# Optimization experiments

Measured on AMD Instinct MI355X. Metric: run time of the kernel, lower is better.

## Reference

```python
import jax, jax.numpy as jnp
import numpy as np

NOISE_LEVEL = 0.02
CROSSTALK = 0.05
COHERENCE = 0.03
HIDDEN = 2048


def _crosstalk_kernel(n):
    # K[i, j] = 1 / (i - j)^2 for i != j, 0 on the diagonal
    idx = jnp.arange(n, dtype=jnp.float32)
    dist = jnp.abs(idx[:, None] - idx[None, :])
    return jnp.where(dist > 0, 1.0 / (dist * dist), 0.0)


def setup_inputs() -> dict:
    key = jax.random.key(0)
    ks = jax.random.split(key, 7)
    B, D_in, H, D_out = 8192, 1024, 2048, 2
    x = jax.random.normal(ks[0], (B, D_in), dtype=jnp.float32)
    # torch nn.Linear-like init scale: 1/sqrt(fan_in)
    W1 = jax.random.normal(ks[1], (H, D_in), dtype=jnp.float32) / np.sqrt(D_in)
    b1 = jax.random.normal(ks[2], (H,), dtype=jnp.float32) / np.sqrt(D_in)
    W2 = jax.random.normal(ks[3], (H, H), dtype=jnp.float32) / np.sqrt(H)
    b2 = jax.random.normal(ks[4], (H,), dtype=jnp.float32) / np.sqrt(H)
    Wout = jax.random.normal(ks[5], (D_out, H), dtype=jnp.float32) / np.sqrt(H)
    bout = jax.random.normal(ks[6], (D_out,), dtype=jnp.float32) / np.sqrt(H)
    return {"x": x, "W1": W1, "b1": b1, "W2": W2, "b2": b2, "Wout": Wout, "bout": bout}


def reference(x, W1, b1, W2, b2, Wout, bout):
    K = _crosstalk_kernel(HIDDEN)
    thermal = jnp.zeros((HIDDEN,), dtype=x.dtype)  # thermal_state buffer, carries across layers
    nkey = jax.random.key(42)

    x = jnp.tanh(x)
    for li, (W, b) in enumerate([(W1, b1), (W2, b2)]):
        x = jnp.tanh(x @ W.T + b)
        # physical noise (add_noise=True, training mode)
        k_noise = jax.random.fold_in(nkey, 2 * li)
        k_phase = jax.random.fold_in(nkey, 2 * li + 1)
        x = x + jax.random.normal(k_noise, x.shape, x.dtype) * NOISE_LEVEL
        # thermal crosstalk: EMA of per-neuron absolute power, then
        # distance-weighted (1/d^2) coupling — the O(n^2) python loop as a matvec
        layer_thermal = jnp.sum(jnp.abs(x), axis=0) * CROSSTALK  # [H]
        thermal = 0.7 * thermal + 0.3 * layer_thermal
        thermal_noise = (thermal @ K) * CROSSTALK  # [H], constant across batch
        x = x + thermal_noise[None, :]
        # coherence (phase-dependent interference)
        phase = jax.random.normal(k_phase, x.shape, x.dtype) * COHERENCE
        x = x + (x * jnp.cos(phase) - x) * COHERENCE
    return x @ Wout.T + bout
```

## Files before the change

### kernel.cpp

```cpp
#include <hip/hip_runtime.h>
#include <stdint.h>
#include <math.h>

#define NOISE_LEVEL 0.02f
#define CROSSTALK   0.05f
#define COHERENCE   0.03f
#define F_COH 0.99998650f

typedef _Float16 half8 __attribute__((ext_vector_type(8)));
typedef _Float16 half4 __attribute__((ext_vector_type(4)));
typedef __attribute__((ext_vector_type(4))) float f32x4;

#define TF_ROUND(x0,x1,R) { x0 += x1; x1 = ((x1 << (R)) | (x1 >> (32-(R)))); x1 ^= x0; }

__host__ __device__ inline void threefry2x32(uint32_t k0, uint32_t k1,
                                             uint32_t x0, uint32_t x1,
                                             uint32_t& o0, uint32_t& o1)
{
  uint32_t ks2 = k0 ^ k1 ^ 0x1BD11BDAu;
  x0 += k0; x1 += k1;
  TF_ROUND(x0,x1,13) TF_ROUND(x0,x1,15) TF_ROUND(x0,x1,26) TF_ROUND(x0,x1,6)
  x0 += k1; x1 += ks2 + 1u;
  TF_ROUND(x0,x1,17) TF_ROUND(x0,x1,29) TF_ROUND(x0,x1,16) TF_ROUND(x0,x1,24)
  x0 += ks2; x1 += k0 + 2u;
  TF_ROUND(x0,x1,13) TF_ROUND(x0,x1,15) TF_ROUND(x0,x1,26) TF_ROUND(x0,x1,6)
  x0 += k0; x1 += k1 + 3u;
  TF_ROUND(x0,x1,17) TF_ROUND(x0,x1,29) TF_ROUND(x0,x1,16) TF_ROUND(x0,x1,24)
  x0 += k1; x1 += ks2 + 4u;
  TF_ROUND(x0,x1,13) TF_ROUND(x0,x1,15) TF_ROUND(x0,x1,26) TF_ROUND(x0,x1,6)
  o0 = x0 + ks2; o1 = x1 + k0 + 5u;
}

__device__ inline uint32_t jax_bits(uint32_t k0, uint32_t k1, uint32_t idx)
{
  uint32_t o0, o1; threefry2x32(k0, k1, 0u, idx, o0, o1); return o0 ^ o1;
}

__device__ inline float jax_normal(uint32_t k0, uint32_t k1, uint32_t idx)
{
  uint32_t bits = jax_bits(k0, k1, idx);
  float f = __uint_as_float((bits >> 9) | 0x3f800000u) - 1.0f;
  float u = fmaf(f, 2.0f, -0.99999994f);
  u = fmaxf(-0.99999994f, u);
  float w = -__logf(fmaf(-u, u, 1.0f));
  float wl = w - 2.5f;
  float p = 2.81022636e-08f;
  p = fmaf(p, wl, 3.43273939e-07f);
  p = fmaf(p, wl, -3.5233877e-06f);
  p = fmaf(p, wl, -4.39150654e-06f);
  p = fmaf(p, wl, 0.00021858087f);
  p = fmaf(p, wl, -0.00125372503f);
  p = fmaf(p, wl, -0.00417768164f);
  p = fmaf(p, wl, 0.246640727f);
  p = fmaf(p, wl, 1.50140941f);
  if (__any(w >= 5.0f)) {
    float ws = sqrtf(w) - 3.0f;
    float q = -0.000200214257f;
    q = fmaf(q, ws, 0.000100950558f);
    q = fmaf(q, ws, 0.00134934322f);
    q = fmaf(q, ws, -0.00367342844f);
    q = fmaf(q, ws, 0.00573950773f);
    q = fmaf(q, ws, -0.0076224613f);
    q = fmaf(q, ws, 0.00943887047f);
    q = fmaf(q, ws, 1.00167406f);
    q = fmaf(q, ws, 2.83297682f);
    p = (w >= 5.0f) ? q : p;
  }
  return 1.41421354f * (p * u);
}

__device__ inline float tanh_fast(float x)
{
  float ax = fabsf(x);
  float e = __expf(2.0f * ax);
  float r = 1.0f - 2.0f / (e + 1.0f);
  return copysignf(r, x);
}

__global__ __launch_bounds__(256)
void pack_plane(const float* __restrict__ in, _Float16* __restrict__ out,
                int R, int K, int kshift, int rbbits, int do_tanh)
{
  const int nslots = R * (K >> 3);
  const int ktm = (K >> 5) - 1;
  const int slotbits = rbbits + 2;
  int g = blockIdx.x * 256 + threadIdx.x;
  const int stride = gridDim.x * 256;
  for (; g < nslots; g += stride) {
    int tile = g >> slotbits;
    int s = g & ((1 << slotbits) - 1);
    int kq = s >> rbbits, row = s & ((1 << rbbits) - 1);
    int rb = tile >> kshift, kt = tile & ktm;
    int r = (rb << rbbits) + row;
    int k = kt * 32 + kq * 8;
    const float* src = in + (size_t)r * K + k;
    float4 v0 = *(const float4*)src;
    float4 v1 = *(const float4*)(src + 4);
    float xs[8] = {v0.x, v0.y, v0.z, v0.w, v1.x, v1.y, v1.z, v1.w};
    half8 h;
    #pragma unroll
    for (int e = 0; e < 8; ++e) {
      float x = do_tanh ? tanh_fast(xs[e]) : xs[e];
      h[e] = (_Float16)x;
    }
    *(half8*)&out[(size_t)g * 8] = h;
  }
}

__device__ __forceinline__ size_t cnat_idx(int r, int c)
{
  int bm = r >> 7, bn = c >> 6, rr = r & 127, cc = c & 63;
  int w = ((rr >> 6) << 1) | (cc >> 5);
  int fm = (rr >> 4) & 3, lg = (rr >> 2) & 3, j = rr & 3;
  int fn = (cc >> 4) & 1, lm = cc & 15;
  return (((size_t)(bm * 32 + bn) * 4 + w) * 32 + fn * 16 + fm * 4 + j) * 64
         + lg * 16 + lm;
}

__global__ __launch_bounds__(256)
void bias_fold(const float* __restrict__ tn, const float* __restrict__ W,
               const float* __restrict__ b, float* __restrict__ fold,
               int K, int nrows, float scale)
{
  const int wid = threadIdx.x >> 6;
  const int lane = threadIdx.x & 63;
  const int j = blockIdx.x * 4 + wid;
  if (j >= nrows) return;
  const float* row = W + (size_t)j * K;
  float s = 0.0f;
  for (int h = lane; h < K; h += 64) s = fmaf(tn[h], row[h], s);
  #pragma unroll
  for (int off = 32; off > 0; off >>= 1) s += __shfl_down(s, off);
  if (lane == 0) fold[j] = fmaf(scale, s, b[j]);
}

#define BM 128
#define BN 64
#define ATILE 4096
#define BTILE 2048
#define BUFH  (ATILE + BTILE)

__device__ __forceinline__ f32x4 noise_group(int g, int blockM, int blockN,
                                             int wr, int wc, int lg, int lm,
                                             int N, uint32_t k0, uint32_t k1)
{
  int fn = g >> 2, fm = g & 3;
  int gr0 = blockM + wr * 64 + fm * 16 + lg * 4;
  int gc  = blockN + wc * 32 + fn * 16 + lm;
  f32x4 r;
  #pragma unroll
  for (int j = 0; j < 4; ++j)
    r[j] = jax_normal(k0, k1, (uint32_t)((gr0 + j) * N + gc));
  return r;
}

template<int OUTMODE>
__global__ __launch_bounds__(256, 5)
void gemm_f16(const _Float16* __restrict__ Ap, const _Float16* __restrict__ Bp,
              const float* __restrict__ bias, _Float16* __restrict__ outn,
              float* __restrict__ colabs, int M, int N, int K, float oscale,
              uint32_t nk0, uint32_t nk1)
{
  __shared__ __align__(16) _Float16 lds[2 * BUFH];

  const int t = threadIdx.x;
  const int bid = blockIdx.x;
  const int xcd = bid & 7, p = bid >> 3;
  const int s = p >> 5, q = p & 31;
  const int bm = ((xcd >> 1) << 4) + ((s >> 1) << 2) + (q >> 3);
  const int bn = ((xcd & 1) << 4) + ((s & 1) << 3) + (q & 7);
  const int blockM = bm * BM, blockN = bn * BN;

  const int lane = t & 63;
  const int w = t >> 6;
  const int wr = w >> 1, wc = w & 1;
  const int lm = lane & 15, lg = lane >> 4;

  const int ktiles = K >> 5;

  const _Float16* gsrc[3];
  int gstride[3];
  _Float16* ldst[3];
  #pragma unroll
  for (int i = 0; i < 3; ++i) {
    int l = w * 3 + i;
    if (l < 8) {
      gsrc[i] = Ap + ((size_t)bm * ktiles) * ATILE + l * 512 + lane * 8;
      gstride[i] = ATILE;
      ldst[i] = lds + l * 512;
    } else {
      gsrc[i] = Bp + ((size_t)bn * ktiles) * BTILE + (l - 8) * 512 + lane * 8;
      gstride[i] = BTILE;
      ldst[i] = lds + ATILE + (l - 8) * 512;
    }
  }

#define STAGE(buf, kt_) {                                                      \
    _Pragma("unroll")                                                          \
    for (int i = 0; i < 3; ++i)                                                \
      __builtin_amdgcn_global_load_lds(                                        \
          (const void*)(gsrc[i] + (size_t)(kt_) * gstride[i]),                 \
          (void*)(ldst[i] + (buf) * BUFH), 16, 0, 0);                          \
  }

  f32x4 acc[4][2];
  #pragma unroll
  for (int i = 0; i < 4; ++i)
    #pragma unroll
    for (int j = 0; j < 2; ++j) acc[i][j] = 0.0f;

  half4 nh0 = 0, nh1 = 0, nh2 = 0, nh3 = 0, nh4 = 0, nh5 = 0, nh6 = 0, nh7 = 0;

  const int nk = ktiles;
  STAGE(0, 0);
  __syncthreads();
  int cur = 0;

  for (int kt = 0; kt < nk; ++kt) {
    if (kt + 1 < nk) STAGE(cur ^ 1, kt + 1);

    const _Float16* base = lds + cur * BUFH;
    half8 fa[4], fb[2];
    #pragma unroll
    for (int fm = 0; fm < 4; ++fm)
      fa[fm] = *(const half8*)(base + lg * 1024 + (wr * 64 + fm * 16 + lm) * 8);
    #pragma unroll
    for (int fn = 0; fn < 2; ++fn)
      fb[fn] = *(const half8*)(base + ATILE + lg * 512 + (wc * 32 + fn * 16 + lm) * 8);
    #pragma unroll
    for (int fm = 0; fm < 4; ++fm)
      #pragma unroll
      for (int fn = 0; fn < 2; ++fn)
        acc[fm][fn] = __builtin_amdgcn_mfma_f32_16x16x32_f16(fa[fm], fb[fn], acc[fm][fn], 0, 0, 0);

    if (kt < 8) {
      f32x4 v = noise_group(kt, blockM, blockN, wr, wc, lg, lm, N, nk0, nk1);
      half4 hv;
      #pragma unroll
      for (int j = 0; j < 4; ++j) hv[j] = (_Float16)v[j];
      switch (kt) {
        case 0: nh0 = hv; break;  case 1: nh1 = hv; break;
        case 2: nh2 = hv; break;  case 3: nh3 = hv; break;
        case 4: nh4 = hv; break;  case 5: nh5 = hv; break;
        case 6: nh6 = hv; break;  default: nh7 = hv; break;
      }
    }

    __syncthreads();
    cur ^= 1;
  }

  const size_t wbase0 = ((size_t)(bm * 64 + bn * 2 + wc)) * 4096
                        + (size_t)(lm >> 3) * 1024 + (lm & 7);
  const size_t obase1 = (((size_t)(bm * 32 + bn) * 4 + w) * 32) * 64 + lane;

#define EPI_STORE(fm_, fn_, NZV)                                               \
    _Pragma("unroll")                                                          \
    for (int j = 0; j < 4; ++j) {                                              \
      float v = tanh_fast(fmaf(oscale, acc[fm_][fn_][j], bv))                  \
                + NOISE_LEVEL * (float)NZV[j];                                 \
      if (OUTMODE == 0)                                                        \
        outn[wbase0 + (fn_)*2048 + (size_t)(wr*64 + (fm_)*16 + lg*4 + j)*8]    \
            = (_Float16)v;                                                     \
      else                                                                     \
        outn[obase1 + (size_t)((fn_)*16 + (fm_)*4 + j) * 64] = (_Float16)v;    \
      cp += fabsf(v);                                                          \
    }

#define EPI_FN(fn_, NZA, NZB, NZC, NZD) {                                      \
    const int gc = blockN + wc * 32 + (fn_)*16 + lm;                           \
    const float bv = bias[gc];                                                 \
    float cp = 0.0f;                                                           \
    EPI_STORE(0, fn_, NZA) EPI_STORE(1, fn_, NZB)                              \
    EPI_STORE(2, fn_, NZC) EPI_STORE(3, fn_, NZD)                              \
    cp += __shfl_xor(cp, 16);                                                  \
    cp += __shfl_xor(cp, 32);                                                  \
    if (lg == 0) atomicAdd(&colabs[gc], cp);                                   \
  }

  EPI_FN(0, nh0, nh1, nh2, nh3)
  EPI_FN(1, nh4, nh5, nh6, nh7)
#undef EPI_FN
#undef EPI_STORE
#undef STAGE
}

__global__ __launch_bounds__(256)
void thermal_tn(const float* __restrict__ colabs, const float* __restrict__ prev_thermal,
                float* __restrict__ thermal_out, float* __restrict__ tn_out, int has_prev)
{
  __shared__ float th[2048];
  __shared__ float inv[2048];
  const int t = threadIdx.x;
  for (int j = t; j < 2048; j += 256) {
    float lt = colabs[j] * CROSSTALK;
    float pv = has_prev ? prev_thermal[j] : 0.0f;
    th[j] = 0.7f * pv + 0.3f * lt;
    float d = (float)j;
    inv[j] = (j == 0) ? 0.0f : 1.0f / (d * d);
  }
  __syncthreads();
  const int i = blockIdx.x * 256 + t;
  float s = 0.0f;
  #pragma unroll 4
  for (int j = 0; j < 2048; ++j) {
    int d = i - j; d = d < 0 ? -d : d;
    s += th[j] * inv[d];
  }
  tn_out[i] = s * CROSSTALK;
  thermal_out[i] = th[i];
}

__global__ __launch_bounds__(256)
void final_out(const _Float16* __restrict__ a2n, const float* __restrict__ Wout,
               const float* __restrict__ foldout, float* __restrict__ out)
{
  const int wave = threadIdx.x >> 6;
  const int lane = threadIdx.x & 63;
  const int b = blockIdx.x * 4 + wave;
  float acc0 = 0.0f, acc1 = 0.0f;
  #pragma unroll
  for (int i = 0; i < 8; ++i) {
    int h = lane * 4 + i * 256;
    half4 v4 = *(const half4*)&a2n[cnat_idx(b, h)];
    float4 w0 = *(const float4*)&Wout[h];
    float4 w1 = *(const float4*)&Wout[2048 + h];
    float xs[4]  = {(float)v4[0], (float)v4[1], (float)v4[2], (float)v4[3]};
    float w0s[4] = {w0.x, w0.y, w0.z, w0.w};
    float w1s[4] = {w1.x, w1.y, w1.z, w1.w};
    #pragma unroll
    for (int e = 0; e < 4; ++e) {
      acc0 = fmaf(xs[e], w0s[e], acc0);
      acc1 = fmaf(xs[e], w1s[e], acc1);
    }
  }
  #pragma unroll
  for (int off = 32; off > 0; off >>= 1) {
    acc0 += __shfl_down(acc0, off);
    acc1 += __shfl_down(acc1, off);
  }
  if (lane == 0) {
    out[(size_t)b * 2 + 0] = fmaf(F_COH, acc0, foldout[0]);
    out[(size_t)b * 2 + 1] = fmaf(F_COH, acc1, foldout[1]);
  }
}

extern "C" void kernel_launch(void* const* d_in, const int* in_sizes, int n_in,
                              void* d_out, int out_size, void* d_ws, size_t ws_size,
                              hipStream_t stream)
{
  (void)in_sizes; (void)n_in; (void)out_size; (void)ws_size;
  const float* x    = (const float*)d_in[0];
  const float* W1   = (const float*)d_in[1];
  const float* b1   = (const float*)d_in[2];
  const float* W2   = (const float*)d_in[3];
  const float* b2   = (const float*)d_in[4];
  const float* Wout = (const float*)d_in[5];
  const float* bout = (const float*)d_in[6];
  float* out = (float*)d_out;

  const int M = 8192, H = 2048, Din = 1024;
  const size_t MB = (size_t)1024 * 1024;

  char* ws = (char*)d_ws;
  _Float16* a2n = (_Float16*)ws;
  _Float16* a1pk = (_Float16*)(ws + 32 * MB);
  _Float16* xpk = (_Float16*)(ws + 64 * MB);
  _Float16* W1p = (_Float16*)(ws + 80 * MB);
  _Float16* W2p = (_Float16*)(ws + 84 * MB);
  float* small = (float*)(ws + 96 * MB);
  float* colabs1  = small + 0 * H;
  float* colabs2  = small + 1 * H;
  float* thermal1 = small + 2 * H;
  float* thermal2 = small + 3 * H;
  float* tn1      = small + 4 * H;
  float* tn2      = small + 5 * H;
  float* foldb    = small + 6 * H;
  float* foldout  = small + 7 * H;

  uint32_t kn0a, kn0b, kn1a, kn1b;
  threefry2x32(0u, 42u, 0u, 0u, kn0a, kn0b);
  threefry2x32(0u, 42u, 0u, 2u, kn1a, kn1b);

  hipMemsetAsync(colabs1, 0, 2 * H * sizeof(float), stream);

  pack_plane<<<1024, 256, 0, stream>>>(W1, W1p, H, Din, 5, 6, 0);
  pack_plane<<<2048, 256, 0, stream>>>(W2, W2p, H, H, 6, 6, 0);
  pack_plane<<<2048, 256, 0, stream>>>(x, xpk, M, Din, 5, 7, 1);

  const int nblk = (M / BM) * (H / BN);
  gemm_f16<0><<<nblk, 256, 0, stream>>>(xpk, W1p, b1, a1pk, colabs1,
                                        M, H, Din, 1.0f, kn0a, kn0b);
  thermal_tn<<<H / 256, 256, 0, stream>>>(colabs1, nullptr, thermal1, tn1, 0);
  bias_fold<<<H / 4, 256, 0, stream>>>(tn1, W2, b2, foldb, H, H, F_COH);
  gemm_f16<1><<<nblk, 256, 0, stream>>>(a1pk, W2p, foldb, a2n, colabs2,
                                        M, H, H, F_COH, kn1a, kn1b);
  thermal_tn<<<H / 256, 256, 0, stream>>>(colabs2, thermal1, thermal2, tn2, 1);
  bias_fold<<<1, 256, 0, stream>>>(tn2, Wout, bout, foldout, H, 2, F_COH);
  final_out<<<M / 4, 256, 0, stream>>>(a2n, Wout, foldout, out);
}
```

Baseline: 360.6 us.

## Stage layer-1 epilogue through swizzled LDS for coalesced stores; merge pack kernels

The first GEMM's epilogue now writes its fp16 outputs into shared memory with an XOR swizzle, then each thread copies them out as 16-byte vectors in the packed layout the next GEMM expects. This replaces scattered 2-byte global stores with coalesced wide stores. The three separate pack launches are also merged into one kernel that picks its source by index range, saving two launches. The cost is an extra barrier, LDS reuse after the main loop (assuming the buffer is large enough and free), and some per-element branching in the pack kernel.

Result: no change. 355.8 us (-1.3%).

```diff
diff --git a/kernel.cpp b/kernel.cpp
--- a/kernel.cpp
+++ b/kernel.cpp
@@ -77,18 +77,29 @@
   return copysignf(r, x);
 }
 
+
 __global__ __launch_bounds__(256)
-void pack_plane(const float* __restrict__ in, _Float16* __restrict__ out,
-                int R, int K, int kshift, int rbbits, int do_tanh)
-{
-  const int nslots = R * (K >> 3);
-  const int ktm = (K >> 5) - 1;
-  const int slotbits = rbbits + 2;
+void pack_all(const float* __restrict__ W1, const float* __restrict__ W2,
+              const float* __restrict__ x,
+              _Float16* __restrict__ W1p, _Float16* __restrict__ W2p,
+              _Float16* __restrict__ xpk)
+{
+  const int n0 = (2048 * 1024) / 8;
+  const int n1 = (2048 * 2048) / 8;
+  const int n2 = (8192 * 1024) / 8;
+  const int total = n0 + n1 + n2;
   int g = blockIdx.x * 256 + threadIdx.x;
   const int stride = gridDim.x * 256;
-  for (; g < nslots; g += stride) {
-    int tile = g >> slotbits;
-    int s = g & ((1 << slotbits) - 1);
+  for (; g < total; g += stride) {
+    const float* in; _Float16* out;
+    int gg, K, kshift, rbbits, do_tanh;
+    if (g < n0)           { in = W1; out = W1p; gg = g;           K = 1024; kshift = 5; rbbits = 6; do_tanh = 0; }
+    else if (g < n0 + n1) { in = W2; out = W2p; gg = g - n0;      K = 2048; kshift = 6; rbbits = 6; do_tanh = 0; }
+    else                  { in = x;  out = xpk; gg = g - n0 - n1; K = 1024; kshift = 5; rbbits = 7; do_tanh = 1; }
+    const int ktm = (K >> 5) - 1;
+    const int slotbits = rbbits + 2;
+    int tile = gg >> slotbits;
+    int s = gg & ((1 << slotbits) - 1);
     int kq = s >> rbbits, row = s & ((1 << rbbits) - 1);
     int rb = tile >> kshift, kt = tile & ktm;
     int r = (rb << rbbits) + row;
@@ -100,10 +111,10 @@
     half8 h;
     #pragma unroll
     for (int e = 0; e < 8; ++e) {
-      float x = do_tanh ? tanh_fast(xs[e]) : xs[e];
-      h[e] = (_Float16)x;
-    }
-    *(half8*)&out[(size_t)g * 8] = h;
+      float xv = do_tanh ? tanh_fast(xs[e]) : xs[e];
+      h[e] = (_Float16)xv;
+    }
+    *(half8*)&out[(size_t)gg * 8] = h;
   }
 }
 
@@ -250,8 +261,6 @@
     cur ^= 1;
   }
 
-  const size_t wbase0 = ((size_t)(bm * 64 + bn * 2 + wc)) * 4096
-                        + (size_t)(lm >> 3) * 1024 + (lm & 7);
   const size_t obase1 = (((size_t)(bm * 32 + bn) * 4 + w) * 32) * 64 + lane;
 
 #define EPI_STORE(fm_, fn_, NZV)                                               \
@@ -259,11 +268,13 @@
     for (int j = 0; j < 4; ++j) {                                              \
       float v = tanh_fast(fmaf(oscale, acc[fm_][fn_][j], bv))                  \
                 + NOISE_LEVEL * (float)NZV[j];                                 \
-      if (OUTMODE == 0)                                                        \
-        outn[wbase0 + (fn_)*2048 + (size_t)(wr*64 + (fm_)*16 + lg*4 + j)*8]    \
-            = (_Float16)v;                                                     \
-      else                                                                     \
+      if (OUTMODE == 0) {                                                      \
+        int R = wr * 64 + (fm_) * 16 + lg * 4 + j;                             \
+        int C = wc * 32 + (fn_) * 16 + lm;                                     \
+        lds[R * 64 + (C ^ ((R & 7) << 3))] = (_Float16)v;                      \
+      } else {                                                                 \
         outn[obase1 + (size_t)((fn_)*16 + (fm_)*4 + j) * 64] = (_Float16)v;    \
+      }                                                                        \
       cp += fabsf(v);                                                          \
     }
 
@@ -280,6 +291,21 @@
 
   EPI_FN(0, nh0, nh1, nh2, nh3)
   EPI_FN(1, nh4, nh5, nh6, nh7)
+
+  if (OUTMODE == 0) {
+    __syncthreads();
+    _Float16* dstb = outn + ((size_t)bm * 64 + 2 * bn) * 4096;
+    #pragma unroll
+    for (int pp = 0; pp < 4; ++pp) {
+      int gidx = pp * 256 + t;
+      int row = gidx & 127;
+      int kq = (gidx >> 7) & 3;
+      int kh = gidx >> 9;
+      int cbase = kh * 32 + kq * 8;
+      half8 hv = *(const half8*)&lds[row * 64 + (cbase ^ ((row & 7) << 3))];
+      *(half8*)&dstb[(size_t)kh * 4096 + kq * 1024 + row * 8] = hv;
+    }
+  }
 #undef EPI_FN
 #undef EPI_STORE
 #undef STAGE
@@ -384,9 +410,7 @@
 
   hipMemsetAsync(colabs1, 0, 2 * H * sizeof(float), stream);
 
-  pack_plane<<<1024, 256, 0, stream>>>(W1, W1p, H, Din, 5, 6, 0);
-  pack_plane<<<2048, 256, 0, stream>>>(W2, W2p, H, H, 6, 6, 0);
-  pack_plane<<<2048, 256, 0, stream>>>(x, xpk, M, Din, 5, 7, 1);
+  pack_all<<<2048, 256, 0, stream>>>(W1, W2, x, W1p, W2p, xpk);
 
   const int nblk = (M / BM) * (H / BN);
   gemm_f16<0><<<nblk, 256, 0, stream>>>(xpk, W1p, b1, a1pk, colabs1,
```
